# Kernel optimization log

Measured on AMD Instinct MI355X. Metric: run time of the kernel, lower is better.

## Reference

```python
import jax, jax.numpy as jnp
import numpy as np

B, C, H, W = 8, 256, 64, 64
M, R, T_EMB = 4, 4, 128


def conv2d(x, w, b, pad):
    y = jax.lax.conv_general_dilated(x, w, (1, 1), [(pad, pad), (pad, pad)],
                                     dimension_numbers=('NCHW', 'OIHW', 'NCHW'))
    return y + b[None, :, None, None]


def grid_sample_zeros(img, grid):
    # img: [C,H,W]; grid: [...,2]; faithful to torch grid_sample(bilinear,
    # zeros padding, align_corners=True): grid[...,0]->x(width), grid[...,1]->y(height).
    Hh, Ww = img.shape[1], img.shape[2]
    gx = (grid[..., 0] + 1.0) * 0.5 * (Ww - 1)
    gy = (grid[..., 1] + 1.0) * 0.5 * (Hh - 1)
    x0 = jnp.floor(gx); y0 = jnp.floor(gy)
    x1 = x0 + 1.0;      y1 = y0 + 1.0
    wx1 = gx - x0; wx0 = 1.0 - wx1
    wy1 = gy - y0; wy0 = 1.0 - wy1

    def gather(yi, xi):
        valid = (yi >= 0) & (yi < Hh) & (xi >= 0) & (xi < Ww)
        yc = jnp.clip(yi, 0, Hh - 1).astype(jnp.int32)
        xc = jnp.clip(xi, 0, Ww - 1).astype(jnp.int32)
        return img[:, yc, xc] * valid.astype(img.dtype)[None]

    out = (gather(y0, x0) * (wy0 * wx0)[None] + gather(y0, x1) * (wy0 * wx1)[None]
           + gather(y1, x0) * (wy1 * wx0)[None] + gather(y1, x1) * (wy1 * wx1)[None])
    return out  # [C, ...]


def setup_inputs() -> dict:
    key = jax.random.key(0)
    ks = jax.random.split(key, 10)
    s = 0.05
    return {
        'F_x': jax.random.normal(ks[0], (B, C, H, W), jnp.float32),
        'F_c': jax.random.normal(ks[1], (B, C, H, W), jnp.float32),
        't': jax.random.uniform(ks[2], (B,), jnp.float32),
        'w_off': jax.random.normal(ks[3], (2 * M, 2 * C, 3, 3), jnp.float32) * s,
        'b_off': jnp.zeros((2 * M,), jnp.float32),
        'w_attn': jax.random.normal(ks[4], (M, 2 * C, 3, 3), jnp.float32) * s,
        'b_attn': jnp.zeros((M,), jnp.float32),
        'Wp': jnp.ones((M, R), jnp.float32) / R,
        'w_fuse': jax.random.normal(ks[5], (C, M * C, 1, 1), jnp.float32) * s,
        'b_fuse': jnp.zeros((C,), jnp.float32),
        'w1': jax.random.normal(ks[6], (1, T_EMB), jnp.float32) * s,
        'b1': jnp.zeros((T_EMB,), jnp.float32),
        'w2': jax.random.normal(ks[7], (T_EMB, 1), jnp.float32) * s,
        'b2': jnp.zeros((1,), jnp.float32),
    }


def reference(F_x, F_c, t, w_off, b_off, w_attn, b_attn, Wp, w_fuse, b_fuse,
              w1, b1, w2, b2):
    Bb, Cc, Hh, Ww = F_x.shape
    Mm, Rr = Wp.shape
    # interleaved stack/permute/reshape in torch == channel concat [F_x; F_c]
    Fs = jnp.concatenate([F_x, F_c], axis=1)                      # [B,2C,H,W]
    offsets = conv2d(Fs, w_off, b_off, 1).reshape(Bb, Mm, 2, Hh, Ww)
    attn = jax.nn.sigmoid(conv2d(Fs, w_attn, b_attn, 1))          # [B,M,H,W]

    ys = jnp.linspace(-1.0, 1.0, Hh)
    xs = jnp.linspace(-1.0, 1.0, Ww)
    base_grid = jnp.stack(jnp.meshgrid(ys, xs, indexing='ij'), -1)  # [H,W,2] (y,x) order
    # base_pts for R=4 (torch meshgrid ij, rows are (y,x))
    bp = jnp.array([[-0.5, -0.5], [-0.5, 0.5], [0.5, -0.5], [0.5, 0.5]], jnp.float32)
    off = jnp.transpose(offsets, (0, 1, 3, 4, 2))                 # [B,M,H,W,2]
    # grid: [B,M,R,H,W,2]; component order kept as in the original code
    grid = base_grid[None, None, None] + bp[None, None, :, None, None, :] + off[:, :, None]

    # sample F_c per batch over all (M,R,H,W) points at once -> [B,C,M,R,H,W]
    samp = jax.vmap(grid_sample_zeros)(F_c, grid)
    head = jnp.einsum('bcmrhw,mr->bmchw', samp, Wp) * attn[:, :, None]
    head = head.reshape(Bb, Mm * Cc, Hh, Ww)
    F_e = conv2d(head, w_fuse, b_fuse, 0)                         # [B,C,H,W]

    alpha = jax.nn.sigmoid(jax.nn.relu(t[:, None] @ w1 + b1) @ w2 + b2)
    alpha = alpha.reshape(Bb, 1, 1, 1)
    F_out = alpha * F_e + (1.0 - alpha) * F_x
    loss_offset = jnp.mean(jnp.abs(offsets))
    return F_out, loss_offset, offsets
```

## Files before the change

kernel.cpp:

```cpp
#include <hip/hip_runtime.h>
#include <hip/hip_bf16.h>

#define Bc   8
#define Cc   256
#define Hc   64
#define Wc   64
#define HWc  4096
#define KDIM 1024

#define LOSS_IDX   8388608
#define OFFS_BASE  8388609

#define XT_OFF     0u
#define HEAD_OFF   33554432u
#define XF8_OFF    67108864u
#define WC8_OFF    75497472u
#define WBF_OFF    100663296u
#define ATTN_OFF   101187584u
#define ALPHA_OFF  101711872u
#define LOSSP_OFF  101712128u
#define WREP_OFF   101714176u
#define ZPAGE_OFF  101935360u

typedef unsigned short u16;
typedef unsigned char u8;
typedef __attribute__((ext_vector_type(8))) short bf16x8;
typedef __attribute__((ext_vector_type(8))) unsigned short u16x8;
typedef __attribute__((ext_vector_type(4))) float f32x4;
typedef __attribute__((ext_vector_type(2))) float f32x2;

#define GLL(gsrc, ldst) __builtin_amdgcn_global_load_lds( \
    (const __attribute__((address_space(1))) unsigned int*)(gsrc), \
    (__attribute__((address_space(3))) unsigned int*)(ldst), 16, 0, 0)

static __device__ __forceinline__ u16 f2bf(float f) {
    unsigned int u = __float_as_uint(f);
    unsigned int r = (u + 0x7FFFu + ((u >> 16) & 1u)) >> 16;
    return (u16)r;
}
static __device__ __forceinline__ float bf2f(u16 h) {
    return __uint_as_float(((unsigned int)h) << 16);
}
static __device__ __forceinline__ unsigned int pk4_fp8(float a, float b, float c, float d) {
    int r = __builtin_amdgcn_cvt_pk_fp8_f32(a, b, 0, false);
    r = __builtin_amdgcn_cvt_pk_fp8_f32(c, d, r, true);
    return (unsigned int)r;
}

__global__ __launch_bounds__(256) void pack_x(
    const float* __restrict__ Fx, const float* __restrict__ Fc,
    u16* __restrict__ Xt, u8* __restrict__ Xlo8, u8* __restrict__ Xf8,
    const float* __restrict__ wf, u8* __restrict__ wf8,
    const float* __restrict__ w_off, const float* __restrict__ w_attn,
    u16* __restrict__ wconv, u8* __restrict__ wconv8, float* __restrict__ zpage) {
    const int tid = threadIdx.x;
    if (blockIdx.x < 2048) {
        const int blk = blockIdx.x;
        const int b = blk >> 8;
        const int rem = blk & 255;
        const int ch0 = (rem >> 6) << 7;
        const int pos0 = (rem & 63) << 6;
        const int cs = (tid & 15) << 3;
        const int p4 = (tid >> 4) << 2;
        const float* basep = (ch0 < 256)
            ? Fx + (((size_t)b << 8) + ch0) * HWc
            : Fc + (((size_t)b << 8) + (ch0 - 256)) * HWc;
        float4 v[8];
#pragma unroll
        for (int k = 0; k < 8; ++k)
            v[k] = *(const float4*)(basep + (size_t)(cs + k) * HWc + pos0 + p4);
#pragma unroll
        for (int j = 0; j < 4; ++j) {
            float w[8];
#pragma unroll
            for (int k = 0; k < 8; ++k) w[k] = ((const float*)&v[k])[j];
            u16x8 hi8;
#pragma unroll
            for (int k = 0; k < 8; ++k) hi8[k] = f2bf(w[k]);
            const size_t row = ((size_t)b << 12) + pos0 + p4 + j;
            *(u16x8*)(Xt + row * 512 + ch0 + cs) = hi8;
            uint2 lo8;
            lo8.x = pk4_fp8((w[0] - bf2f(hi8[0])) * 256.f, (w[1] - bf2f(hi8[1])) * 256.f,
                            (w[2] - bf2f(hi8[2])) * 256.f, (w[3] - bf2f(hi8[3])) * 256.f);
            lo8.y = pk4_fp8((w[4] - bf2f(hi8[4])) * 256.f, (w[5] - bf2f(hi8[5])) * 256.f,
                            (w[6] - bf2f(hi8[6])) * 256.f, (w[7] - bf2f(hi8[7])) * 256.f);
            *(uint2*)(Xlo8 + row * 512 + ch0 + cs) = lo8;
            if (ch0 >= 256) {
                uint2 f8;
                f8.x = pk4_fp8(w[0], w[1], w[2], w[3]);
                f8.y = pk4_fp8(w[4], w[5], w[6], w[7]);
                *(uint2*)(Xf8 + row * 256 + (ch0 - 256) + cs) = f8;
            }
        }
    } else if (blockIdx.x < 2304) {
        const int i = (blockIdx.x - 2048) * 256 + tid;
        const float4 v = *(const float4*)(wf + (size_t)i * 4);
        *(unsigned int*)(wf8 + (size_t)i * 4) = pk4_fp8(v.x, v.y, v.z, v.w);
    } else if (blockIdx.x < 2312) {
        const int step = blockIdx.x - 2304;
        for (int n = tid; n < 1728; n += 256) {
            const int par = n & 1;
            const int slot = (n >> 1) & 3;
            const int pair = (n >> 3) % 6;
            const int tap = (n / 48) % 9;
            const int prec = (n / 432) & 1;
            const int sub = n / 864;
            const int oc = pair * 2 + par;
            const int c = slot ^ (pair & 3);
            const int ch = step * 64 + sub * 32 + c * 8;
            u16x8 out;
#pragma unroll
            for (int j = 0; j < 8; ++j) {
                const float v = (oc < 8)
                    ? w_off[((size_t)oc * 512 + ch + j) * 9 + tap]
                    : w_attn[((size_t)(oc - 8) * 512 + ch + j) * 9 + tap];
                const u16 h = f2bf(v);
                out[j] = prec ? f2bf(v - bf2f(h)) : h;
            }
            *(u16x8*)(wconv + ((size_t)step * 1728 + n) * 8) = out;
        }
        for (int n = tid; n < 1152; n += 256) {
            const int slot = n & 3;
            const int oc = (n >> 2) & 15;
            const int tap = (n >> 6) % 9;
            const int sub = n / 576;
            const int g = slot ^ (oc >> 2);
            const int ch = step * 64 + sub * 32 + g * 8;
            float v[8];
#pragma unroll
            for (int j = 0; j < 8; ++j)
                v[j] = (oc < 8) ? w_off[((size_t)oc * 512 + ch + j) * 9 + tap]
                     : (oc < 12) ? w_attn[((size_t)(oc - 8) * 512 + ch + j) * 9 + tap] : 0.f;
            uint2 o;
            o.x = pk4_fp8(v[0], v[1], v[2], v[3]);
            o.y = pk4_fp8(v[4], v[5], v[6], v[7]);
            *(uint2*)(wconv8 + (size_t)step * 9216 + n * 8) = o;
        }
    } else {
        if (tid < 64) zpage[tid] = 0.f;
    }
}

__global__ __launch_bounds__(512) void conv_mfma(
    const u16* __restrict__ Xt, const u8* __restrict__ Xlo8,
    const u16* __restrict__ wconv, const u8* __restrict__ wconv8,
    const float* __restrict__ zpage,
    const float* __restrict__ b_off, const float* __restrict__ b_attn,
    float* __restrict__ dout, float* __restrict__ attnb, float* __restrict__ lossp) {
    __shared__ char smem[138240];

    const int tid = threadIdx.x;
    const int wv = tid >> 6, lane = tid & 63;
    const int gp = wv >> 2, qd = wv & 3;
    const int l15 = lane & 15, g = lane >> 4;
    const int b = blockIdx.x >> 5;
    const int h0 = (blockIdx.x & 31) * 2;
    const int wrow = qd >> 1, wcol0 = (qd & 1) * 32;

    if (tid < 192) {
        const float4 z = {0.f, 0.f, 0.f, 0.f};
        if (tid < 128) {
            const int bu = tid >> 6, rr = (tid >> 4) & 3, hp = (tid >> 3) & 1, cc = tid & 7;
            *(float4*)(smem + bu * 33792 + rr * 8448 + (hp ? 65 : 0) * 128 + cc * 16) = z;
        } else {
            const int t2 = tid - 128;
            const int bu = t2 >> 5, rr = (t2 >> 3) & 3, hp = (t2 >> 2) & 1, cc = t2 & 3;
            *(float4*)(smem + 67584 + bu * 16896 + rr * 4224 + (hp ? 65 : 0) * 64 + cc * 16) = z;
        }
    }

    int pre[2][3], plo[2][3];
#pragma unroll
    for (int f = 0; f < 2; ++f)
#pragma unroll
        for (int dx = 0; dx < 3; ++dx) {
            const int p = wcol0 + f * 16 + l15 + dx;
            pre[f][dx] = wrow * 8448 + p * 128 + ((((gp << 2) | g) ^ (p & 7)) << 4);
            const int cl = (gp * 2 + (g >> 1)) ^ ((p & 3) ^ ((p >> 2) & 3));
            plo[f][dx] = 67584 + wrow * 4224 + p * 64 + cl * 16 + (g & 1) * 8;
        }
    const int bpair = l15 >> 1, bpar = l15 & 1;
    const int vb = 101376 + gp * 13824 + bpair * 128 + ((g ^ (bpair & 3)) << 5) + bpar * 16;
    const int vb8 = 129024 + gp * 4608 + l15 * 32 + ((g ^ (l15 >> 2)) << 3);

    auto stage_X = [&](int step, int buf) {
#pragma unroll
        for (int k = 0; k < 7; ++k) {
            const int f = wv * 7 + k;
            if (f < 36) {
                const int rr = f / 9, i = f % 9;
                const int p = i * 8 + (lane >> 3);
                const int c = (lane & 7) ^ (p & 7);
                const int h = h0 - 1 + rr;
                const bool act = (p >= 1) && (p <= 64);
                const char* gsrc = (h >= 0 && h < 64)
                    ? (const char*)(Xt + (((size_t)((b << 12) + h * 64 + p - 1)) << 9) + step * 64 + c * 8)
                    : (const char*)zpage + ((lane & 7) << 4);
                char* ldst = smem + buf * 33792 + rr * 8448 + i * 1024;
                if (act) GLL(gsrc, ldst);
            } else {
                const int f2 = f - 36;
                const int rr = f2 / 5, i = f2 % 5;
                const int p = i * 16 + (lane >> 2);
                const int c = (lane & 3) ^ ((p & 3) ^ ((p >> 2) & 3));
                const int h = h0 - 1 + rr;
                const bool act = (p >= 1) && (p <= 64);
                const char* gsrc = (h >= 0 && h < 64)
                    ? (const char*)(Xlo8 + (((size_t)((b << 12) + h * 64 + p - 1)) << 9) + step * 64 + c * 16)
                    : (const char*)zpage + ((lane & 3) << 4);
                char* ldst = smem + 67584 + buf * 16896 + rr * 4224 + i * 1024;
                if (act) GLL(gsrc, ldst);
            }
        }
    };
    auto stage_B = [&](int step) {
        for (int i = wv; i < 36; i += 8) {
            if (i < 27) {
                const char* gsrc = (const char*)wconv + (((size_t)step * 1728) + i * 64 + lane) * 16;
                GLL(gsrc, smem + 101376 + i * 1024);
            } else {
                const int j = i - 27;
                const char* gsrc = (const char*)wconv8 + (size_t)step * 9216 + j * 1024 + lane * 16;
                GLL(gsrc, smem + 129024 + j * 1024);
            }
        }
    };

    __syncthreads();
    stage_X(0, 0);
    stage_B(0);
    __syncthreads();

    f32x4 acc0 = {}, acc1 = {}, al0 = {}, al1 = {};

    for (int step = 0; step < 8; ++step) {
        if (step < 7) {
            stage_X(step + 1, (step + 1) & 1);
            asm volatile("s_waitcnt vmcnt(7)" ::: "memory");
        } else {
            asm volatile("s_waitcnt vmcnt(0)" ::: "memory");
        }
        __builtin_amdgcn_s_barrier();
        __builtin_amdgcn_sched_barrier(0);

#pragma unroll
        for (int tap = 0; tap < 9; ++tap) {
            const int dy = tap / 3, dx = tap % 3;
            const bf16x8 bh = *(const bf16x8*)(smem + vb + tap * 768);
            const bf16x8 bl = *(const bf16x8*)(smem + vb + 6912 + tap * 768);
            const long b8 = *(const long*)(smem + vb8 + tap * 512);
            const bf16x8 a0h = *(const bf16x8*)(smem + pre[0][dx] + dy * 8448);
            const bf16x8 a1h = *(const bf16x8*)(smem + pre[1][dx] + dy * 8448);
            const long a0l = *(const long*)(smem + plo[0][dx] + dy * 4224);
            const long a1l = *(const long*)(smem + plo[1][dx] + dy * 4224);
            acc0 = __builtin_amdgcn_mfma_f32_16x16x32_bf16(a0h, bh, acc0, 0, 0, 0);
            acc1 = __builtin_amdgcn_mfma_f32_16x16x32_bf16(a1h, bh, acc1, 0, 0, 0);
            acc0 = __builtin_amdgcn_mfma_f32_16x16x32_bf16(a0h, bl, acc0, 0, 0, 0);
            acc1 = __builtin_amdgcn_mfma_f32_16x16x32_bf16(a1h, bl, acc1, 0, 0, 0);
            al0 = __builtin_amdgcn_mfma_f32_16x16x32_fp8_fp8(a0l, b8, al0, 0, 0, 0);
            al1 = __builtin_amdgcn_mfma_f32_16x16x32_fp8_fp8(a1l, b8, al1, 0, 0, 0);
        }

        __builtin_amdgcn_sched_barrier(0);
        __builtin_amdgcn_s_barrier();
        __builtin_amdgcn_sched_barrier(0);
        if (step < 7) stage_B(step + 1);
        const int dh = (step & 1) ? -33792 : 33792;
        const int dl = (step & 1) ? -16896 : 16896;
#pragma unroll
        for (int f = 0; f < 2; ++f)
#pragma unroll
            for (int dx = 0; dx < 3; ++dx) { pre[f][dx] += dh; plo[f][dx] += dl; }
    }

    __syncthreads();
    float* eL = (float*)smem;
    if (l15 < 12) {
#pragma unroll
        for (int r = 0; r < 4; ++r) {
            const int px0 = wrow * 64 + wcol0 + g * 4 + r;
            eL[(gp * 12 + l15) * 128 + px0] = acc0[r] + al0[r] * (1.f / 256.f);
            eL[(gp * 12 + l15) * 128 + px0 + 16] = acc1[r] + al1[r] * (1.f / 256.f);
        }
    }
    __syncthreads();
    float labs = 0.f;
    if (tid < 256) {
        const int oc = tid >> 5, seg = tid & 31;
        const float4 v0 = *(const float4*)&eL[oc * 128 + seg * 4];
        const float4 v1 = *(const float4*)&eL[(12 + oc) * 128 + seg * 4];
        const float bo = b_off[oc];
        float4 o;
        o.x = v0.x + v1.x + bo; o.y = v0.y + v1.y + bo;
        o.z = v0.z + v1.z + bo; o.w = v0.w + v1.w + bo;
        *(float4*)(dout + OFFS_BASE + (((size_t)b * 8 + oc) << 12) + h0 * 64 + seg * 4) = o;
        labs = fabsf(o.x) + fabsf(o.y) + fabsf(o.z) + fabsf(o.w);
    } else if (tid < 384) {
        const int t2 = tid - 256;
        const int oc = t2 >> 5, seg = t2 & 31;
        const float4 v0 = *(const float4*)&eL[(8 + oc) * 128 + seg * 4];
        const float4 v1 = *(const float4*)&eL[(20 + oc) * 128 + seg * 4];
        const float ba = b_attn[oc];
        float4 o;
        o.x = 1.f / (1.f + expf(-(v0.x + v1.x + ba)));
        o.y = 1.f / (1.f + expf(-(v0.y + v1.y + ba)));
        o.z = 1.f / (1.f + expf(-(v0.z + v1.z + ba)));
        o.w = 1.f / (1.f + expf(-(v0.w + v1.w + ba)));
        *(float4*)(attnb + (((size_t)b * 4 + oc) << 12) + h0 * 64 + seg * 4) = o;
    }
#pragma unroll
    for (int off = 32; off; off >>= 1) labs += __shfl_down(labs, off);
    float* wr = (float*)(smem + 14336);
    if (lane == 0) wr[wv] = labs;
    __syncthreads();
    if (tid == 0) {
        float s = 0.f;
#pragma unroll
        for (int i = 0; i < 8; ++i) s += wr[i];
        lossp[blockIdx.x] = s;
    }
}

__global__ __launch_bounds__(256) void finalize_small(
    const float* __restrict__ lossp, const float* __restrict__ t,
    const float* __restrict__ w1, const float* __restrict__ b1,
    const float* __restrict__ w2, const float* __restrict__ b2,
    float* __restrict__ dout, float* __restrict__ alpha) {
    __shared__ float sd[4];
    const int tid = threadIdx.x;
    float s = lossp[tid];
#pragma unroll
    for (int off = 32; off; off >>= 1) s += __shfl_down(s, off);
    if ((tid & 63) == 0) sd[tid >> 6] = s;
    __syncthreads();
    if (tid == 0) dout[LOSS_IDX] = (sd[0] + sd[1] + sd[2] + sd[3]) * (1.f / 262144.f);

    for (int b = 0; b < 8; ++b) {
        __syncthreads();
        float v = 0.f;
        if (tid < 128) v = fmaxf(fmaf(t[b], w1[tid], b1[tid]), 0.f) * w2[tid];
#pragma unroll
        for (int off = 32; off; off >>= 1) v += __shfl_down(v, off);
        if ((tid & 63) == 0) sd[tid >> 6] = v;
        __syncthreads();
        if (tid == 0) alpha[b] = 1.f / (1.f + expf(-(sd[0] + sd[1] + b2[0])));
    }
}

__global__ __launch_bounds__(256) void sample_head(
    const u8* __restrict__ Xf8, const float* __restrict__ dout,
    const float* __restrict__ attnb, const float* __restrict__ Wp,
    u8* __restrict__ head) {
    const int tid = threadIdx.x;
    const int wv = tid >> 6, lane = tid & 63;
    const int item = blockIdx.x * 4 + wv;
    const int b = item >> 14;
    const int m = (item >> 12) & 3;
    const int p = item & 4095;
    const int h = p >> 6, wc = p & 63;
    const int hl = lane >> 5, l32 = lane & 31;

    const float off0 = dout[OFFS_BASE + (((size_t)b * 8 + 2 * m) << 12) + p];
    const float off1 = dout[OFFS_BASE + (((size_t)b * 8 + 2 * m + 1) << 12) + p];
    const float a    = attnb[(((size_t)b * 4 + m) << 12) + p];

    const float ysh = -1.f + h * (2.f / 63.f);
    const float xsw = -1.f + wc * (2.f / 63.f);

    const u8* base = Xf8 + (((size_t)b << 12) << 8) + l32 * 8;
    float acc[8] = {};

#pragma unroll
    for (int r = 0; r < 4; ++r) {
        const float bpy = (r < 2) ? -0.5f : 0.5f;
        const float bpx = (r & 1) ? 0.5f : -0.5f;
        const float c0 = ysh + bpy + off0;
        const float c1 = xsw + bpx + off1;
        const float ix = (c0 + 1.f) * 31.5f;
        const float iy = (c1 + 1.f) * 31.5f;
        const float x0 = floorf(ix), y0 = floorf(iy);
        const float wx1 = ix - x0, wx0 = 1.f - wx1;
        const float wy1 = iy - y0, wy0 = 1.f - wy1;
        const float xf = x0 + hl;
        const float wxl = (hl ? wx1 : wx0) * (Wp[m * 4 + r] * a);
        const bool xin = (xf >= 0.f) && (xf < 64.f);
        const bool v0 = xin && (y0 >= 0.f) && (y0 < 64.f);
        const bool v1 = xin && (y0 >= -1.f) && (y0 < 63.f);
        const int xi = (int)xf;
        uint2 u0, u1;
        if (v0) u0 = *(const uint2*)(base + ((size_t)((((int)y0) << 6) + xi)) * 256);
        if (v1) u1 = *(const uint2*)(base + ((size_t)((((int)y0 + 1) << 6) + xi)) * 256);
        if (v0) {
            const float w = wxl * wy0;
            const f32x2 pa = __builtin_amdgcn_cvt_pk_f32_fp8((int)u0.x, false);
            const f32x2 pb = __builtin_amdgcn_cvt_pk_f32_fp8((int)u0.x, true);
            const f32x2 pc = __builtin_amdgcn_cvt_pk_f32_fp8((int)u0.y, false);
            const f32x2 pd = __builtin_amdgcn_cvt_pk_f32_fp8((int)u0.y, true);
            acc[0] = fmaf(w, pa[0], acc[0]); acc[1] = fmaf(w, pa[1], acc[1]);
            acc[2] = fmaf(w, pb[0], acc[2]); acc[3] = fmaf(w, pb[1], acc[3]);
            acc[4] = fmaf(w, pc[0], acc[4]); acc[5] = fmaf(w, pc[1], acc[5]);
            acc[6] = fmaf(w, pd[0], acc[6]); acc[7] = fmaf(w, pd[1], acc[7]);
        }
        if (v1) {
            const float w = wxl * wy1;
            const f32x2 pa = __builtin_amdgcn_cvt_pk_f32_fp8((int)u1.x, false);
            const f32x2 pb = __builtin_amdgcn_cvt_pk_f32_fp8((int)u1.x, true);
            const f32x2 pc = __builtin_amdgcn_cvt_pk_f32_fp8((int)u1.y, false);
            const f32x2 pd = __builtin_amdgcn_cvt_pk_f32_fp8((int)u1.y, true);
            acc[0] = fmaf(w, pa[0], acc[0]); acc[1] = fmaf(w, pa[1], acc[1]);
            acc[2] = fmaf(w, pb[0], acc[2]); acc[3] = fmaf(w, pb[1], acc[3]);
            acc[4] = fmaf(w, pc[0], acc[4]); acc[5] = fmaf(w, pc[1], acc[5]);
            acc[6] = fmaf(w, pd[0], acc[6]); acc[7] = fmaf(w, pd[1], acc[7]);
        }
    }
#pragma unroll
    for (int j = 0; j < 8; ++j) acc[j] += __shfl_xor(acc[j], 32);
    if (lane < 32) {
        uint2 o;
        o.x = pk4_fp8(acc[0], acc[1], acc[2], acc[3]);
        o.y = pk4_fp8(acc[4], acc[5], acc[6], acc[7]);
        *(uint2*)(head + ((((size_t)b << 12) + p)) * KDIM + m * 256 + l32 * 8) = o;
    }
}

__global__ __launch_bounds__(256) void fuse_gemm(
    const u8* __restrict__ head, const u8* __restrict__ wf8,
    const float* __restrict__ Fx, const float* __restrict__ bfuse,
    const float* __restrict__ alpha, float* __restrict__ dout) {
    __shared__ __attribute__((aligned(16))) char smem[2][2][8192];

    const int tid = threadIdx.x;
    const int lane = tid & 63, wv = tid >> 6;
    const int wm = wv >> 1, wn = wv & 1;
    const int l15 = lane & 15, g = lane >> 4;
    const size_t arow0 = (size_t)blockIdx.x * 128;
    const int co0 = blockIdx.y * 128;

    f32x4 acc[4][4] = {};

    const int isB = wv >> 1;
    const int whalf = wv & 1;
    const u8* srcbase = isB ? wf8 + (size_t)co0 * KDIM : head + arow0 * KDIM;

    auto stage = [&](int kt, int buf) {
#pragma unroll
        for (int i = 0; i < 4; ++i) {
            const int row = whalf * 64 + i * 16 + (lane >> 2);
            const int gq = (lane & 3) ^ ((row >> 1) & 3);
            const u8* gsrc = srcbase + (size_t)row * KDIM + kt * 64 + gq * 16;
            char* ldst = smem[buf][isB] + (whalf * 64 + i * 16) * 64;
            GLL(gsrc, ldst);
        }
    };

    stage(0, 0);
    __syncthreads();

    for (int kt = 0; kt < 16; ++kt) {
        if (kt < 15) {
            stage(kt + 1, (kt + 1) & 1);
            asm volatile("s_waitcnt vmcnt(4)" ::: "memory");
        } else {
            asm volatile("s_waitcnt vmcnt(0)" ::: "memory");
        }
        __builtin_amdgcn_s_barrier();
        __builtin_amdgcn_sched_barrier(0);

        const char* Ab = smem[kt & 1][0];
        const char* Bb = smem[kt & 1][1];
#pragma unroll
        for (int s = 0; s < 2; ++s) {
            const int gg = s * 4 + g;
            long av[4], bv[4];
#pragma unroll
            for (int f = 0; f < 4; ++f) {
                const int ra = wm * 64 + f * 16 + l15;
                const int rb = wn * 64 + f * 16 + l15;
                const int sa = (gg >> 1) ^ ((ra >> 1) & 3);
                const int sb = (gg >> 1) ^ ((rb >> 1) & 3);
                av[f] = *(const long*)(Ab + ra * 64 + sa * 16 + (gg & 1) * 8);
                bv[f] = *(const long*)(Bb + rb * 64 + sb * 16 + (gg & 1) * 8);
            }
#pragma unroll
            for (int i = 0; i < 4; ++i)
#pragma unroll
                for (int j = 0; j < 4; ++j)
                    acc[i][j] = __builtin_amdgcn_mfma_f32_16x16x32_fp8_fp8(av[i], bv[j], acc[i][j], 0, 0, 0);
        }

        __builtin_amdgcn_sched_barrier(0);
        __builtin_amdgcn_s_barrier();
        __builtin_amdgcn_sched_barrier(0);
    }

    const int b = (int)(arow0 >> 12);
    const float al = alpha[b], il = 1.f - al;
    const int pixbase = (int)(arow0 & 4095);
#pragma unroll
    for (int i = 0; i < 4; ++i) {
        const int rowl = wm * 64 + i * 16 + g * 4;
        const int pix = pixbase + rowl;
#pragma unroll
        for (int j = 0; j < 4; ++j) {
            const int co = co0 + wn * 64 + j * 16 + l15;
            const float bias = bfuse[co];
            const size_t idx = (((size_t)b << 8) + co) * HWc + pix;
            const float4 fx = *(const float4*)(Fx + idx);
            const f32x4 v = acc[i][j];
            float4 o;
            o.x = al * (v[0] + bias) + il * fx.x;
            o.y = al * (v[1] + bias) + il * fx.y;
            o.z = al * (v[2] + bias) + il * fx.z;
            o.w = al * (v[3] + bias) + il * fx.w;
            *(float4*)(dout + idx) = o;
        }
    }
}

extern "C" void kernel_launch(void* const* d_in, const int* in_sizes, int n_in,
                              void* d_out, int out_size, void* d_ws, size_t ws_size,
                              hipStream_t stream) {
    const float* F_x    = (const float*)d_in[0];
    const float* F_c    = (const float*)d_in[1];
    const float* t      = (const float*)d_in[2];
    const float* w_off  = (const float*)d_in[3];
    const float* b_off  = (const float*)d_in[4];
    const float* w_attn = (const float*)d_in[5];
    const float* b_attn = (const float*)d_in[6];
    const float* Wp     = (const float*)d_in[7];
    const float* w_fuse = (const float*)d_in[8];
    const float* b_fuse = (const float*)d_in[9];
    const float* w1     = (const float*)d_in[10];
    const float* b1     = (const float*)d_in[11];
    const float* w2     = (const float*)d_in[12];
    const float* b2     = (const float*)d_in[13];
    float* out = (float*)d_out;

    char* ws = (char*)d_ws;
    u16*   Xt     = (u16*)(ws + XT_OFF);
    u8*    Xlo8   = (u8*)(ws + HEAD_OFF);
    u8*    head8  = (u8*)(ws + HEAD_OFF);
    u8*    Xf8    = (u8*)(ws + XF8_OFF);
    u8*    wconv8 = (u8*)(ws + WC8_OFF);
    u8*    wf8    = (u8*)(ws + WBF_OFF);
    float* attnb  = (float*)(ws + ATTN_OFF);
    float* alphb  = (float*)(ws + ALPHA_OFF);
    float* lossp  = (float*)(ws + LOSSP_OFF);
    u16*   wconv  = (u16*)(ws + WREP_OFF);
    float* zpage  = (float*)(ws + ZPAGE_OFF);

    pack_x<<<dim3(2313), dim3(256), 0, stream>>>(F_x, F_c, Xt, Xlo8, Xf8,
                                                 w_fuse, wf8, w_off, w_attn,
                                                 wconv, wconv8, zpage);
    conv_mfma<<<dim3(256), dim3(512), 0, stream>>>(Xt, Xlo8, wconv, wconv8, zpage,
                                                   b_off, b_attn, out, attnb, lossp);
    finalize_small<<<dim3(1), dim3(256), 0, stream>>>(lossp, t, w1, b1, w2, b2, out, alphb);
    sample_head<<<dim3(32768), dim3(256), 0, stream>>>(Xf8, out, attnb, Wp, head8);
    fuse_gemm<<<dim3(256, 2), dim3(256), 0, stream>>>(head8, wf8, F_x, b_fuse, alphb, out);
}
```

Baseline: 124.4 us.

## Switch offset/attn conv from bf16+fp8 split to fp16 with scaled weight residual

The 3x3 offset/attention convolution previously split activations into a bf16 high part plus an fp8 residual and ran extra fp8 MFMAs. It now stores activations as fp16 only and splits just the weights into an fp16 high part and a 512-scaled fp16 residual, using f16 MFMAs. This drops the activation residual pack/store, its staging into LDS, and the fp8 weight copy, which shrinks LDS use and global traffic. The cost is lower activation precision and possible fp16 range issues, so offset accuracy depends on the inputs staying in range.

```diff
diff --git a/kernel.cpp b/kernel.cpp
--- a/kernel.cpp
+++ b/kernel.cpp
@@ -1,5 +1,6 @@
 #include <hip/hip_runtime.h>
 #include <hip/hip_bf16.h>
+#include <hip/hip_fp16.h>
 
 #define Bc   8
 #define Cc   256
@@ -14,7 +15,6 @@
 #define XT_OFF     0u
 #define HEAD_OFF   33554432u
 #define XF8_OFF    67108864u
-#define WC8_OFF    75497472u
 #define WBF_OFF    100663296u
 #define ATTN_OFF   101187584u
 #define ALPHA_OFF  101711872u
@@ -24,7 +24,7 @@
 
 typedef unsigned short u16;
 typedef unsigned char u8;
-typedef __attribute__((ext_vector_type(8))) short bf16x8;
+typedef __attribute__((ext_vector_type(8))) _Float16 f16x8;
 typedef __attribute__((ext_vector_type(8))) unsigned short u16x8;
 typedef __attribute__((ext_vector_type(4))) float f32x4;
 typedef __attribute__((ext_vector_type(2))) float f32x2;
@@ -33,13 +33,13 @@
     (const __attribute__((address_space(1))) unsigned int*)(gsrc), \
     (__attribute__((address_space(3))) unsigned int*)(ldst), 16, 0, 0)
 
-static __device__ __forceinline__ u16 f2bf(float f) {
-    unsigned int u = __float_as_uint(f);
-    unsigned int r = (u + 0x7FFFu + ((u >> 16) & 1u)) >> 16;
-    return (u16)r;
-}
-static __device__ __forceinline__ float bf2f(u16 h) {
-    return __uint_as_float(((unsigned int)h) << 16);
+static __device__ __forceinline__ u16 f2h(float f) {
+    __half h = __float2half(f);
+    return *(u16*)&h;
+}
+static __device__ __forceinline__ float h2f(u16 u) {
+    __half h = *(__half*)&u;
+    return __half2float(h);
 }
 static __device__ __forceinline__ unsigned int pk4_fp8(float a, float b, float c, float d) {
     int r = __builtin_amdgcn_cvt_pk_fp8_f32(a, b, 0, false);
@@ -49,10 +49,10 @@
 
 __global__ __launch_bounds__(256) void pack_x(
     const float* __restrict__ Fx, const float* __restrict__ Fc,
-    u16* __restrict__ Xt, u8* __restrict__ Xlo8, u8* __restrict__ Xf8,
+    u16* __restrict__ Xt, u8* __restrict__ Xf8,
     const float* __restrict__ wf, u8* __restrict__ wf8,
     const float* __restrict__ w_off, const float* __restrict__ w_attn,
-    u16* __restrict__ wconv, u8* __restrict__ wconv8, float* __restrict__ zpage) {
+    u16* __restrict__ wconv, float* __restrict__ zpage) {
     const int tid = threadIdx.x;
     if (blockIdx.x < 2048) {
         const int blk = blockIdx.x;
@@ -76,15 +76,9 @@
             for (int k = 0; k < 8; ++k) w[k] = ((const float*)&v[k])[j];
             u16x8 hi8;
 #pragma unroll
-            for (int k = 0; k < 8; ++k) hi8[k] = f2bf(w[k]);
+            for (int k = 0; k < 8; ++k) hi8[k] = f2h(w[k]);
             const size_t row = ((size_t)b << 12) + pos0 + p4 + j;
             *(u16x8*)(Xt + row * 512 + ch0 + cs) = hi8;
-            uint2 lo8;
-            lo8.x = pk4_fp8((w[0] - bf2f(hi8[0])) * 256.f, (w[1] - bf2f(hi8[1])) * 256.f,
-                            (w[2] - bf2f(hi8[2])) * 256.f, (w[3] - bf2f(hi8[3])) * 256.f);
-            lo8.y = pk4_fp8((w[4] - bf2f(hi8[4])) * 256.f, (w[5] - bf2f(hi8[5])) * 256.f,
-                            (w[6] - bf2f(hi8[6])) * 256.f, (w[7] - bf2f(hi8[7])) * 256.f);
-            *(uint2*)(Xlo8 + row * 512 + ch0 + cs) = lo8;
             if (ch0 >= 256) {
                 uint2 f8;
                 f8.x = pk4_fp8(w[0], w[1], w[2], w[3]);
@@ -114,40 +108,23 @@
                 const float v = (oc < 8)
                     ? w_off[((size_t)oc * 512 + ch + j) * 9 + tap]
                     : w_attn[((size_t)(oc - 8) * 512 + ch + j) * 9 + tap];
-                const u16 h = f2bf(v);
-                out[j] = prec ? f2bf(v - bf2f(h)) : h;
+                const u16 h = f2h(v);
+                out[j] = prec ? f2h((v - h2f(h)) * 512.f) : h;
             }
             *(u16x8*)(wconv + ((size_t)step * 1728 + n) * 8) = out;
         }
-        for (int n = tid; n < 1152; n += 256) {
-            const int slot = n & 3;
-            const int oc = (n >> 2) & 15;
-            const int tap = (n >> 6) % 9;
-            const int sub = n / 576;
-            const int g = slot ^ (oc >> 2);
-            const int ch = step * 64 + sub * 32 + g * 8;
-            float v[8];
-#pragma unroll
-            for (int j = 0; j < 8; ++j)
-                v[j] = (oc < 8) ? w_off[((size_t)oc * 512 + ch + j) * 9 + tap]
-                     : (oc < 12) ? w_attn[((size_t)(oc - 8) * 512 + ch + j) * 9 + tap] : 0.f;
-            uint2 o;
-            o.x = pk4_fp8(v[0], v[1], v[2], v[3]);
-            o.y = pk4_fp8(v[4], v[5], v[6], v[7]);
-            *(uint2*)(wconv8 + (size_t)step * 9216 + n * 8) = o;
-        }
     } else {
         if (tid < 64) zpage[tid] = 0.f;
     }
 }
 
+#define B_BASE 67584
 __global__ __launch_bounds__(512) void conv_mfma(
-    const u16* __restrict__ Xt, const u8* __restrict__ Xlo8,
-    const u16* __restrict__ wconv, const u8* __restrict__ wconv8,
-    const float* __restrict__ zpage,
+    const u16* __restrict__ Xt,
+    const u16* __restrict__ wconv, const float* __restrict__ zpage,
     const float* __restrict__ b_off, const float* __restrict__ b_attn,
     float* __restrict__ dout, float* __restrict__ attnb, float* __restrict__ lossp) {
-    __shared__ char smem[138240];
+    __shared__ char smem[95232];
 
     const int tid = threadIdx.x;
     const int wv = tid >> 6, lane = tid & 63;
@@ -157,36 +134,27 @@
     const int h0 = (blockIdx.x & 31) * 2;
     const int wrow = qd >> 1, wcol0 = (qd & 1) * 32;
 
-    if (tid < 192) {
+    if (tid < 128) {
         const float4 z = {0.f, 0.f, 0.f, 0.f};
-        if (tid < 128) {
-            const int bu = tid >> 6, rr = (tid >> 4) & 3, hp = (tid >> 3) & 1, cc = tid & 7;
-            *(float4*)(smem + bu * 33792 + rr * 8448 + (hp ? 65 : 0) * 128 + cc * 16) = z;
-        } else {
-            const int t2 = tid - 128;
-            const int bu = t2 >> 5, rr = (t2 >> 3) & 3, hp = (t2 >> 2) & 1, cc = t2 & 3;
-            *(float4*)(smem + 67584 + bu * 16896 + rr * 4224 + (hp ? 65 : 0) * 64 + cc * 16) = z;
-        }
-    }
-
-    int pre[2][3], plo[2][3];
+        const int bu = tid >> 6, rr = (tid >> 4) & 3, hp = (tid >> 3) & 1, cc = tid & 7;
+        *(float4*)(smem + bu * 33792 + rr * 8448 + (hp ? 65 : 0) * 128 + cc * 16) = z;
+    }
+
+    int pre[2][3];
 #pragma unroll
     for (int f = 0; f < 2; ++f)
 #pragma unroll
         for (int dx = 0; dx < 3; ++dx) {
             const int p = wcol0 + f * 16 + l15 + dx;
             pre[f][dx] = wrow * 8448 + p * 128 + ((((gp << 2) | g) ^ (p & 7)) << 4);
-            const int cl = (gp * 2 + (g >> 1)) ^ ((p & 3) ^ ((p >> 2) & 3));
-            plo[f][dx] = 67584 + wrow * 4224 + p * 64 + cl * 16 + (g & 1) * 8;
         }
     const int bpair = l15 >> 1, bpar = l15 & 1;
-    const int vb = 101376 + gp * 13824 + bpair * 128 + ((g ^ (bpair & 3)) << 5) + bpar * 16;
-    const int vb8 = 129024 + gp * 4608 + l15 * 32 + ((g ^ (l15 >> 2)) << 3);
+    const int vb = B_BASE + gp * 13824 + bpair * 128 + ((g ^ (bpair & 3)) << 5) + bpar * 16;
 
     auto stage_X = [&](int step, int buf) {
 #pragma unroll
-        for (int k = 0; k < 7; ++k) {
-            const int f = wv * 7 + k;
+        for (int k = 0; k < 5; ++k) {
+            const int f = k * 8 + wv;
             if (f < 36) {
                 const int rr = f / 9, i = f % 9;
                 const int p = i * 8 + (lane >> 3);
@@ -198,31 +166,13 @@
                     : (const char*)zpage + ((lane & 7) << 4);
                 char* ldst = smem + buf * 33792 + rr * 8448 + i * 1024;
                 if (act) GLL(gsrc, ldst);
-            } else {
-                const int f2 = f - 36;
-                const int rr = f2 / 5, i = f2 % 5;
-                const int p = i * 16 + (lane >> 2);
-                const int c = (lane & 3) ^ ((p & 3) ^ ((p >> 2) & 3));
-                const int h = h0 - 1 + rr;
-                const bool act = (p >= 1) && (p <= 64);
-                const char* gsrc = (h >= 0 && h < 64)
-                    ? (const char*)(Xlo8 + (((size_t)((b << 12) + h * 64 + p - 1)) << 9) + step * 64 + c * 16)
-                    : (const char*)zpage + ((lane & 3) << 4);
-                char* ldst = smem + 67584 + buf * 16896 + rr * 4224 + i * 1024;
-                if (act) GLL(gsrc, ldst);
             }
         }
     };
     auto stage_B = [&](int step) {
-        for (int i = wv; i < 36; i += 8) {
-            if (i < 27) {
-                const char* gsrc = (const char*)wconv + (((size_t)step * 1728) + i * 64 + lane) * 16;
-                GLL(gsrc, smem + 101376 + i * 1024);
-            } else {
-                const int j = i - 27;
-                const char* gsrc = (const char*)wconv8 + (size_t)step * 9216 + j * 1024 + lane * 16;
-                GLL(gsrc, smem + 129024 + j * 1024);
-            }
+        for (int i = wv; i < 27; i += 8) {
+            const char* gsrc = (const char*)wconv + (((size_t)step * 1728) + i * 64 + lane) * 16;
+            GLL(gsrc, smem + B_BASE + i * 1024);
         }
     };
 
@@ -231,12 +181,13 @@
     stage_B(0);
     __syncthreads();
 
-    f32x4 acc0 = {}, acc1 = {}, al0 = {}, al1 = {};
+    f32x4 acc0 = {}, acc1 = {}, aL0 = {}, aL1 = {};
 
     for (int step = 0; step < 8; ++step) {
         if (step < 7) {
             stage_X(step + 1, (step + 1) & 1);
-            asm volatile("s_waitcnt vmcnt(7)" ::: "memory");
+            if (wv < 4) asm volatile("s_waitcnt vmcnt(5)" ::: "memory");
+            else        asm volatile("s_waitcnt vmcnt(4)" ::: "memory");
         } else {
             asm volatile("s_waitcnt vmcnt(0)" ::: "memory");
         }
@@ -246,19 +197,14 @@
 #pragma unroll
         for (int tap = 0; tap < 9; ++tap) {
             const int dy = tap / 3, dx = tap % 3;
-            const bf16x8 bh = *(const bf16x8*)(smem + vb + tap * 768);
-            const bf16x8 bl = *(const bf16x8*)(smem + vb + 6912 + tap * 768);
-            const long b8 = *(const long*)(smem + vb8 + tap * 512);
-            const bf16x8 a0h = *(const bf16x8*)(smem + pre[0][dx] + dy * 8448);
-            const bf16x8 a1h = *(const bf16x8*)(smem + pre[1][dx] + dy * 8448);
-            const long a0l = *(const long*)(smem + plo[0][dx] + dy * 4224);
-            const long a1l = *(const long*)(smem + plo[1][dx] + dy * 4224);
-            acc0 = __builtin_amdgcn_mfma_f32_16x16x32_bf16(a0h, bh, acc0, 0, 0, 0);
-            acc1 = __builtin_amdgcn_mfma_f32_16x16x32_bf16(a1h, bh, acc1, 0, 0, 0);
-            acc0 = __builtin_amdgcn_mfma_f32_16x16x32_bf16(a0h, bl, acc0, 0, 0, 0);
-            acc1 = __builtin_amdgcn_mfma_f32_16x16x32_bf16(a1h, bl, acc1, 0, 0, 0);
-            al0 = __builtin_amdgcn_mfma_f32_16x16x32_fp8_fp8(a0l, b8, al0, 0, 0, 0);
-            al1 = __builtin_amdgcn_mfma_f32_16x16x32_fp8_fp8(a1l, b8, al1, 0, 0, 0);
+            const f16x8 bh = *(const f16x8*)(smem + vb + tap * 768);
+            const f16x8 bl = *(const f16x8*)(smem + vb + 6912 + tap * 768);
+            const f16x8 a0 = *(const f16x8*)(smem + pre[0][dx] + dy * 8448);
+            const f16x8 a1 = *(const f16x8*)(smem + pre[1][dx] + dy * 8448);
+            acc0 = __builtin_amdgcn_mfma_f32_16x16x32_f16(a0, bh, acc0, 0, 0, 0);
+            acc1 = __builtin_amdgcn_mfma_f32_16x16x32_f16(a1, bh, acc1, 0, 0, 0);
+            aL0  = __builtin_amdgcn_mfma_f32_16x16x32_f16(a0, bl, aL0, 0, 0, 0);
+            aL1  = __builtin_amdgcn_mfma_f32_16x16x32_f16(a1, bl, aL1, 0, 0, 0);
         }
 
         __builtin_amdgcn_sched_barrier(0);
@@ -266,11 +212,10 @@
         __builtin_amdgcn_sched_barrier(0);
         if (step < 7) stage_B(step + 1);
         const int dh = (step & 1) ? -33792 : 33792;
-        const int dl = (step & 1) ? -16896 : 16896;
 #pragma unroll
         for (int f = 0; f < 2; ++f)
 #pragma unroll
-            for (int dx = 0; dx < 3; ++dx) { pre[f][dx] += dh; plo[f][dx] += dl; }
+            for (int dx = 0; dx < 3; ++dx) pre[f][dx] += dh;
     }
 
     __syncthreads();
@@ -279,8 +224,8 @@
 #pragma unroll
         for (int r = 0; r < 4; ++r) {
             const int px0 = wrow * 64 + wcol0 + g * 4 + r;
-            eL[(gp * 12 + l15) * 128 + px0] = acc0[r] + al0[r] * (1.f / 256.f);
-            eL[(gp * 12 + l15) * 128 + px0 + 16] = acc1[r] + al1[r] * (1.f / 256.f);
+            eL[(gp * 12 + l15) * 128 + px0] = acc0[r] + aL0[r] * (1.f / 512.f);
+            eL[(gp * 12 + l15) * 128 + px0 + 16] = acc1[r] + aL1[r] * (1.f / 512.f);
         }
     }
     __syncthreads();
@@ -538,10 +483,8 @@
 
     char* ws = (char*)d_ws;
     u16*   Xt     = (u16*)(ws + XT_OFF);
-    u8*    Xlo8   = (u8*)(ws + HEAD_OFF);
     u8*    head8  = (u8*)(ws + HEAD_OFF);
     u8*    Xf8    = (u8*)(ws + XF8_OFF);
-    u8*    wconv8 = (u8*)(ws + WC8_OFF);
     u8*    wf8    = (u8*)(ws + WBF_OFF);
     float* attnb  = (float*)(ws + ATTN_OFF);
     float* alphb  = (float*)(ws + ALPHA_OFF);
@@ -549,10 +492,10 @@
     u16*   wconv  = (u16*)(ws + WREP_OFF);
     float* zpage  = (float*)(ws + ZPAGE_OFF);
 
-    pack_x<<<dim3(2313), dim3(256), 0, stream>>>(F_x, F_c, Xt, Xlo8, Xf8,
+    pack_x<<<dim3(2313), dim3(256), 0, stream>>>(F_x, F_c, Xt, Xf8,
                                                  w_fuse, wf8, w_off, w_attn,
-                                                 wconv, wconv8, zpage);
-    conv_mfma<<<dim3(256), dim3(512), 0, stream>>>(Xt, Xlo8, wconv, wconv8, zpage,
+                                                 wconv, zpage);
+    conv_mfma<<<dim3(256), dim3(512), 0, stream>>>(Xt, wconv, zpage,
                                                    b_off, b_attn, out, attnb, lossp);
     finalize_small<<<dim3(1), dim3(256), 0, stream>>>(lossp, t, w1, b1, w2, b2, out, alphb);
     sample_head<<<dim3(32768), dim3(256), 0, stream>>>(Xf8, out, attnb, Wp, head8);
```

After: 104.6 us. 15.9% less time.
